# Kernel tuning notes

Measured on AMD Instinct MI355X. Metric: run time of the kernel, lower is better.

## Reference

```python
import jax, jax.numpy as jnp
import numpy as np

B, LQ, LKV = 4, 512, 8192
Q_DIM, KV_DIM = 1024, 512
QK_CH, V_CH, N_HEADS = 256, 256, 8
EPS = 1e-5


def _layernorm(x, g, b):
    m = jnp.mean(x, axis=-1, keepdims=True)
    v = jnp.mean(jnp.square(x - m), axis=-1, keepdims=True)
    return (x - m) * jax.lax.rsqrt(v + EPS) * g + b


def setup_inputs() -> dict:
    key = jax.random.key(0)
    ks = jax.random.split(key, 8)
    hidden_states = jax.random.normal(ks[0], (B, LQ, Q_DIM), dtype=jnp.float32)
    inputs = jax.random.normal(ks[1], (B, LKV, KV_DIM), dtype=jnp.float32)
    # Linear weights stored as [in, out] for x @ W
    Wq = jax.random.normal(ks[2], (Q_DIM, QK_CH), dtype=jnp.float32) * (1.0 / np.sqrt(Q_DIM))
    Wk = jax.random.normal(ks[3], (KV_DIM, QK_CH), dtype=jnp.float32) * (1.0 / np.sqrt(KV_DIM))
    Wv = jax.random.normal(ks[4], (KV_DIM, V_CH), dtype=jnp.float32) * (1.0 / np.sqrt(KV_DIM))
    bq = jnp.zeros((QK_CH,), jnp.float32)
    bk = jax.random.normal(ks[5], (QK_CH,), dtype=jnp.float32) * 0.02
    bv = jax.random.normal(ks[6], (V_CH,), dtype=jnp.float32) * 0.02
    ln1_g = jnp.ones((Q_DIM,), jnp.float32)
    ln1_b = jnp.zeros((Q_DIM,), jnp.float32)
    ln2_g = jnp.ones((KV_DIM,), jnp.float32)
    ln2_b = jnp.zeros((KV_DIM,), jnp.float32)
    return dict(hidden_states=hidden_states, inputs=inputs,
                ln1_g=ln1_g, ln1_b=ln1_b, ln2_g=ln2_g, ln2_b=ln2_b,
                Wq=Wq, bq=bq, Wk=Wk, bk=bk, Wv=Wv, bv=bv)


def reference(hidden_states, inputs, ln1_g, ln1_b, ln2_g, ln2_b,
              Wq, bq, Wk, bk, Wv, bv):
    H = N_HEADS
    dqk = QK_CH // H
    dv = V_CH // H
    hs = _layernorm(hidden_states, ln1_g, ln1_b)          # [B,LQ,Q_DIM]
    inp = _layernorm(inputs, ln2_g, ln2_b)                # [B,LKV,KV_DIM]
    q = (hs @ Wq + bq).reshape(B, LQ, H, dqk)             # [B,LQ,H,dqk]
    k = (inp @ Wk + bk).reshape(B, LKV, H, dqk)           # [B,LKV,H,dqk]
    v = (inp @ Wv + bv).reshape(B, LKV, H, dv)            # [B,LKV,H,dv]
    scores = jnp.einsum('bqhd,bkhd->bhqk', q, k) / np.sqrt(dqk).astype(np.float32)
    probs = jax.nn.softmax(scores, axis=-1)               # [B,H,LQ,LKV] (materialized, as in torch)
    ctx = jnp.einsum('bhqk,bkhd->bqhd', probs, v)         # [B,LQ,H,dv]
    return ctx.reshape(B, LQ, H * dv)
```

## Files before the change

### kernel.cpp

```cpp
#include <hip/hip_runtime.h>
#include <hip/hip_bf16.h>
#include <math.h>

#define NB    4
#define LQ    512
#define LKV   8192
#define QDIM  1024
#define KVDIM 512
#define NH    8
#define EPS_LN 1e-5f
#define SMAX  12.0f

typedef __attribute__((ext_vector_type(8))) short bf16x8;
typedef __attribute__((ext_vector_type(4))) float f32x4;

static __device__ __forceinline__ ushort f2bf(float x) {
    unsigned int u = __builtin_bit_cast(unsigned int, x);
    u += 0x7FFFu + ((u >> 16) & 1u);
    return (ushort)(u >> 16);
}

#if __has_builtin(__builtin_amdgcn_cvt_pk_bf16_f32)
static __device__ __forceinline__ unsigned int pk_bf16(float a, float b) {
    auto r = __builtin_amdgcn_cvt_pk_bf16_f32(a, b);
    return __builtin_bit_cast(unsigned int, r);
}
#else
static __device__ __forceinline__ unsigned int pk_bf16(float a, float b) {
    return (unsigned int)f2bf(a) | ((unsigned int)f2bf(b) << 16);
}
#endif

#if __has_builtin(__builtin_amdgcn_exp2f)
#define EXP2F(x) __builtin_amdgcn_exp2f(x)
#else
#define EXP2F(x) exp2f(x)
#endif

static __device__ __forceinline__ void gld_lds16(const ushort* g, ushort* l) {
    __builtin_amdgcn_global_load_lds(
        (const __attribute__((address_space(1))) unsigned int*)g,
        (__attribute__((address_space(3))) unsigned int*)l, 16, 0, 0);
}

static __device__ __forceinline__ void wt_transpose_body(
    const float* __restrict__ src, ushort* __restrict__ dst, int K,
    int kx, int ny, int t, ushort (*Ts)[72])
{
    const int k0 = kx * 64, n0 = ny * 64;
    const int nl = t & 63;
#pragma unroll
    for (int p = 0; p < 16; ++p) {
        const int kl = p * 4 + (t >> 6);
        Ts[nl][kl] = f2bf(src[(size_t)(k0 + kl) * 256 + n0 + nl]);
    }
    __syncthreads();
    const int ck = (t & 7) * 8;
#pragma unroll
    for (int p = 0; p < 2; ++p) {
        const int rn = p * 32 + (t >> 3);
        *(bf16x8*)(dst + (size_t)(n0 + rn) * K + k0 + ck) = *(const bf16x8*)&Ts[rn][ck];
    }
}

__global__ __launch_bounds__(256) void phaseA_kernel(
    const float* __restrict__ inputs, float* __restrict__ mean_i, float* __restrict__ rstd_i,
    const float* __restrict__ hidden, float* __restrict__ mean_h, float* __restrict__ rstd_h,
    const float* __restrict__ Wq, const float* __restrict__ Wk, const float* __restrict__ Wv,
    ushort* __restrict__ WtQ, ushort* __restrict__ WtKV)
{
    __shared__ ushort Ts[64][72];
    const int bid = blockIdx.x;
    const int t = threadIdx.x;
    const int lane = t & 63;
    if (bid < 8192) {
        const int row = bid * 4 + (t >> 6);
        const float* xp = inputs + (size_t)row * KVDIM;
        float s = 0.f, ss = 0.f;
#pragma unroll
        for (int i = 0; i < 2; ++i) {
            const float4 v = *(const float4*)(xp + lane * 4 + i * 256);
            s  += (v.x + v.y) + (v.z + v.w);
            ss += (v.x * v.x + v.y * v.y) + (v.z * v.z + v.w * v.w);
        }
#pragma unroll
        for (int o = 1; o < 64; o <<= 1) { s += __shfl_xor(s, o, 64); ss += __shfl_xor(ss, o, 64); }
        if (lane == 0) {
            const float mu = s * (1.0f / KVDIM);
            mean_i[row] = mu;
            rstd_i[row] = rsqrtf(ss * (1.0f / KVDIM) - mu * mu + EPS_LN);
        }
    } else if (bid < 8704) {
        const int row = (bid - 8192) * 4 + (t >> 6);
        const float* xp = hidden + (size_t)row * QDIM;
        float s = 0.f, ss = 0.f;
#pragma unroll
        for (int i = 0; i < 4; ++i) {
            const float4 v = *(const float4*)(xp + lane * 4 + i * 256);
            s  += (v.x + v.y) + (v.z + v.w);
            ss += (v.x * v.x + v.y * v.y) + (v.z * v.z + v.w * v.w);
        }
#pragma unroll
        for (int o = 1; o < 64; o <<= 1) { s += __shfl_xor(s, o, 64); ss += __shfl_xor(ss, o, 64); }
        if (lane == 0) {
            const float mu = s * (1.0f / QDIM);
            mean_h[row] = mu;
            rstd_h[row] = rsqrtf(ss * (1.0f / QDIM) - mu * mu + EPS_LN);
        }
    } else if (bid < 8768) {
        const int p = bid - 8704;
        wt_transpose_body(Wq, WtQ, QDIM, p & 15, p >> 4, t, Ts);
    } else if (bid < 8800) {
        const int p = bid - 8768;
        wt_transpose_body(Wk, WtKV, KVDIM, p & 7, p >> 3, t, Ts);
    } else {
        const int p = bid - 8800;
        wt_transpose_body(Wv, WtKV + (size_t)256 * KVDIM, KVDIM, p & 7, p >> 3, t, Ts);
    }
}

__global__ __launch_bounds__(256) void phaseB_kernel(
    const float* __restrict__ inputs,
    const float* __restrict__ mean_i, const float* __restrict__ rstd_i,
    const float* __restrict__ ln2g, const float* __restrict__ ln2b,
    const ushort* __restrict__ WtKV,
    const float* __restrict__ bk, const float* __restrict__ bv,
    ushort* __restrict__ kb, ushort* __restrict__ vt,
    const float* __restrict__ hidden,
    const float* __restrict__ mean_h, const float* __restrict__ rstd_h,
    const float* __restrict__ ln1g, const float* __restrict__ ln1b,
    const ushort* __restrict__ WtQ, const float* __restrict__ bq,
    ushort* __restrict__ qb, float oscale)
{
    __shared__ __align__(16) ushort SMEM[4 * 64 * 72];
    const int bid  = blockIdx.x;
    const int t    = threadIdx.x;
    const int lane = t & 63;
    const int w    = t >> 6;
    const int lq   = lane & 15;
    const int lg   = lane >> 4;
    const int wm   = w >> 1;
    const int wn   = w & 1;

    if (bid < 1024) {
        const int x  = bid & 7;
        const int j  = bid >> 3;
        const int bm = (x * 32 + (j >> 2)) * 128;
        const int bn = (j & 3) * 128;
        ushort* As = SMEM;
        ushort* Bs = SMEM + 4096;

        const int srow = t >> 2;
        const int scol = ((t & 3) ^ ((t >> 3) & 3)) * 8;
        const ushort* gB = WtKV + (size_t)(bn + srow) * KVDIM + scol;
        ushort* lB  = Bs + t * 8;
        ushort* lA0 = As + t * 8;
        ushort* lA1 = As + 2048 + t * 8;

        const int r0 = bm + srow;
        const float rs0 = rstd_i[r0],      mr0 = -mean_i[r0] * rs0;
        const float rs1 = rstd_i[r0 + 64], mr1 = -mean_i[r0 + 64] * rs1;
        const float* xp0 = inputs + (size_t)r0 * KVDIM + scol;
        const float* xp1 = xp0 + (size_t)64 * KVDIM;

        float4 a0 = *(const float4*)(xp0);
        float4 a1 = *(const float4*)(xp0 + 4);
        float4 c0 = *(const float4*)(xp1);
        float4 c1 = *(const float4*)(xp1 + 4);
        float4 g0 = *(const float4*)(ln2g + scol);
        float4 g1 = *(const float4*)(ln2g + scol + 4);
        float4 e0 = *(const float4*)(ln2b + scol);
        float4 e1 = *(const float4*)(ln2b + scol + 4);

        f32x4 acc[4][4] = {};
        for (int k0 = 0; k0 < KVDIM; k0 += 32) {
            gld_lds16(gB + k0,                       lB);
            gld_lds16(gB + (size_t)64 * KVDIM + k0,  lB + 2048);
            uint4 w0, w1;
            w0.x = pk_bf16(fmaf(fmaf(a0.x, rs0, mr0), g0.x, e0.x), fmaf(fmaf(a0.y, rs0, mr0), g0.y, e0.y));
            w0.y = pk_bf16(fmaf(fmaf(a0.z, rs0, mr0), g0.z, e0.z), fmaf(fmaf(a0.w, rs0, mr0), g0.w, e0.w));
            w0.z = pk_bf16(fmaf(fmaf(a1.x, rs0, mr0), g1.x, e1.x), fmaf(fmaf(a1.y, rs0, mr0), g1.y, e1.y));
            w0.w = pk_bf16(fmaf(fmaf(a1.z, rs0, mr0), g1.z, e1.z), fmaf(fmaf(a1.w, rs0, mr0), g1.w, e1.w));
            w1.x = pk_bf16(fmaf(fmaf(c0.x, rs1, mr1), g0.x, e0.x), fmaf(fmaf(c0.y, rs1, mr1), g0.y, e0.y));
            w1.y = pk_bf16(fmaf(fmaf(c0.z, rs1, mr1), g0.z, e0.z), fmaf(fmaf(c0.w, rs1, mr1), g0.w, e0.w));
            w1.z = pk_bf16(fmaf(fmaf(c1.x, rs1, mr1), g1.x, e1.x), fmaf(fmaf(c1.y, rs1, mr1), g1.y, e1.y));
            w1.w = pk_bf16(fmaf(fmaf(c1.z, rs1, mr1), g1.z, e1.z), fmaf(fmaf(c1.w, rs1, mr1), g1.w, e1.w));
            *(uint4*)lA0 = w0;
            *(uint4*)lA1 = w1;
            const int nk = (k0 + 32 < KVDIM) ? k0 + 32 : 0;
            a0 = *(const float4*)(xp0 + nk);
            a1 = *(const float4*)(xp0 + nk + 4);
            c0 = *(const float4*)(xp1 + nk);
            c1 = *(const float4*)(xp1 + nk + 4);
            g0 = *(const float4*)(ln2g + nk + scol);
            g1 = *(const float4*)(ln2g + nk + scol + 4);
            e0 = *(const float4*)(ln2b + nk + scol);
            e1 = *(const float4*)(ln2b + nk + scol + 4);
            __syncthreads();
            bf16x8 af[4], bf[4];
#pragma unroll
            for (int mt = 0; mt < 4; ++mt) {
                const int m = wm * 64 + mt * 16 + lq;
                af[mt] = *(const bf16x8*)(As + m * 32 + ((lg ^ ((m >> 1) & 3)) << 3));
            }
#pragma unroll
            for (int nt = 0; nt < 4; ++nt) {
                const int n = wn * 64 + nt * 16 + lq;
                bf[nt] = *(const bf16x8*)(Bs + n * 32 + ((lg ^ ((n >> 1) & 3)) << 3));
            }
#pragma unroll
            for (int mt = 0; mt < 4; ++mt)
#pragma unroll
                for (int nt = 0; nt < 4; ++nt)
                    acc[mt][nt] = __builtin_amdgcn_mfma_f32_16x16x32_bf16(af[mt], bf[nt], acc[mt][nt], 0, 0, 0);
            __syncthreads();
        }

        const int m0base = bm + wm * 64;
        const int bidx   = m0base >> 13;
        const int tokb   = m0base & 8191;

        if (bn < 256) {
            ushort (*Cs)[72] = (ushort(*)[72])(SMEM + w * 64 * 72);
#pragma unroll
            for (int nt = 0; nt < 4; ++nt) {
                const int n_l = nt * 16 + lq;
                const float bias = bk[bn + wn * 64 + n_l];
#pragma unroll
                for (int mt = 0; mt < 4; ++mt)
#pragma unroll
                    for (int r = 0; r < 4; ++r)
                        Cs[mt * 16 + lg * 4 + r][n_l] = f2bf(acc[mt][nt][r] + bias);
            }
            const int r0_ = lane >> 3;
            const int ck  = (lane & 7) * 8;
            const int nc  = bn + wn * 64 + ck;
            const int h = nc >> 5, d = nc & 31;
            const size_t obase = (((size_t)(bidx * NH + h) << 13) + tokb) * 32 + d;
#pragma unroll
            for (int p = 0; p < 8; ++p) {
                const int row = p * 8 + r0_;
                *(bf16x8*)(kb + obase + (size_t)row * 32) = *(const bf16x8*)&Cs[row][ck];
            }
        } else {
            ushort (*Cs)[72] = (ushort(*)[72])(SMEM + w * 64 * 72);
#pragma unroll
            for (int nt = 0; nt < 4; ++nt) {
                const int n_l = nt * 16 + lq;
                const float bias = bv[(bn - 256) + wn * 64 + n_l];
#pragma unroll
                for (int mt = 0; mt < 4; ++mt) {
                    uint2 o;
                    o.x = pk_bf16(acc[mt][nt][0] + bias, acc[mt][nt][1] + bias);
                    o.y = pk_bf16(acc[mt][nt][2] + bias, acc[mt][nt][3] + bias);
                    *(uint2*)&Cs[n_l][mt * 16 + lg * 4] = o;
                }
            }
            const int r0_ = lane >> 3;
            const int cm  = (lane & 7) * 8;
            const int tokc = tokb + cm;
#pragma unroll
            for (int p = 0; p < 8; ++p) {
                const int row = p * 8 + r0_;
                const int nv  = (bn - 256) + wn * 64 + row;
                const int h = nv >> 5, d = nv & 31;
                *(bf16x8*)(vt + ((size_t)(bidx * NH + h) * 32 + d) * LKV + tokc) =
                    *(const bf16x8*)&Cs[row][cm];
            }
        }
    } else {
        const int p  = bid - 1024;
        const int x  = p & 7;
        const int j  = p >> 3;
        const int bm = (x * 8 + (j >> 2)) * 32;
        const int bn = (j & 3) * 64;
        ushort* As = SMEM;
        ushort* Bs = SMEM + 2048;

        const int srow = t >> 3;
        const int scol = ((t & 7) ^ (srow & 7)) * 8;
        const ushort* gB = WtQ + (size_t)(bn + srow) * QDIM + scol;
        ushort* lB = Bs + t * 8;
        ushort* lA = As + t * 8;

        const int r = bm + srow;
        const float rs0 = rstd_h[r], mr0 = -mean_h[r] * rs0;
        const float* xA = hidden + (size_t)r * QDIM + scol;

        float4 a0 = *(const float4*)(xA);
        float4 a1 = *(const float4*)(xA + 4);
        float4 g0 = *(const float4*)(ln1g + scol);
        float4 g1 = *(const float4*)(ln1g + scol + 4);
        float4 e0 = *(const float4*)(ln1b + scol);
        float4 e1 = *(const float4*)(ln1b + scol + 4);

        f32x4 acc[2] = {};
        for (int k0 = 0; k0 < QDIM; k0 += 64) {
            gld_lds16(gB + k0,                      lB);
            gld_lds16(gB + (size_t)32 * QDIM + k0,  lB + 2048);
            uint4 w0;
            w0.x = pk_bf16(fmaf(fmaf(a0.x, rs0, mr0), g0.x, e0.x), fmaf(fmaf(a0.y, rs0, mr0), g0.y, e0.y));
            w0.y = pk_bf16(fmaf(fmaf(a0.z, rs0, mr0), g0.z, e0.z), fmaf(fmaf(a0.w, rs0, mr0), g0.w, e0.w));
            w0.z = pk_bf16(fmaf(fmaf(a1.x, rs0, mr0), g1.x, e1.x), fmaf(fmaf(a1.y, rs0, mr0), g1.y, e1.y));
            w0.w = pk_bf16(fmaf(fmaf(a1.z, rs0, mr0), g1.z, e1.z), fmaf(fmaf(a1.w, rs0, mr0), g1.w, e1.w));
            *(uint4*)lA = w0;
            const int nk = (k0 + 64 < QDIM) ? k0 + 64 : 0;
            a0 = *(const float4*)(xA + nk);
            a1 = *(const float4*)(xA + nk + 4);
            g0 = *(const float4*)(ln1g + nk + scol);
            g1 = *(const float4*)(ln1g + nk + scol + 4);
            e0 = *(const float4*)(ln1b + nk + scol);
            e1 = *(const float4*)(ln1b + nk + scol + 4);
            __syncthreads();
#pragma unroll
            for (int kh = 0; kh < 2; ++kh) {
                const int m = wm * 16 + lq;
                const bf16x8 af = *(const bf16x8*)(As + m * 64 + (((lg + 4 * kh) ^ (m & 7)) << 3));
#pragma unroll
                for (int nt = 0; nt < 2; ++nt) {
                    const int n = wn * 32 + nt * 16 + lq;
                    const bf16x8 bf = *(const bf16x8*)(Bs + n * 64 + (((lg + 4 * kh) ^ (n & 7)) << 3));
                    acc[nt] = __builtin_amdgcn_mfma_f32_16x16x32_bf16(af, bf, acc[nt], 0, 0, 0);
                }
            }
            __syncthreads();
        }

#pragma unroll
        for (int nt = 0; nt < 2; ++nt) {
            const int n = bn + wn * 32 + nt * 16 + lq;
            const int h = n >> 5, d = n & 31;
            const float bias = bq[n];
            const int m0   = bm + wm * 16 + lg * 4;
            const int bidx = m0 >> 9;
            const int tok  = m0 & 511;
            const size_t base = (((size_t)(bidx * NH + h) << 9) + tok) * 32 + d;
#pragma unroll
            for (int rr_ = 0; rr_ < 4; ++rr_)
                qb[base + (size_t)rr_ * 32] = f2bf((acc[nt][rr_] + bias) * oscale);
        }
    }
}

__global__ __launch_bounds__(512, 4) void attn_mfma_kernel(
    const ushort* __restrict__ Qb,
    const ushort* __restrict__ Kb,
    const ushort* __restrict__ Vt,
    float* __restrict__ Out)
{
    const int bid = blockIdx.x;
    const int xcd = bid & 7;
    const int rr  = bid >> 3;
    const int bh  = ((rr & 3) << 3) | xcd;
    const int qt  = rr >> 2;
    const int b = bh >> 3, h = bh & 7;
    const int t = threadIdx.x, w = t >> 6, lane = t & 63;
    const int lq = lane & 15, lg = lane >> 4;

    __shared__ __align__(16) ushort Pb[2][8][32][40];
    __shared__ float lbuf[8][32];

    bf16x8 qfrag[2];
    const size_t qbase = ((size_t)bh * LQ + qt * 32) * 32;
    qfrag[0] = *(const bf16x8*)(Qb + qbase + (size_t)lq * 32 + lg * 8);
    qfrag[1] = *(const bf16x8*)(Qb + qbase + (size_t)(16 + lq) * 32 + lg * 8);

    const ushort* KpA = Kb + ((size_t)bh * LKV + w * 1024 + lq) * 32 + lg * 8;
    const ushort* VpA = Vt + ((size_t)bh * 32 + lq) * LKV + w * 1024 + lg * 8;

    f32x4 oacc[2][2] = {};
    float l_part[2] = {0.f, 0.f};
    const f32x4 cM = {-SMAX, -SMAX, -SMAX, -SMAX};

    ushort* P0 = &Pb[0][w][0][0];
    ushort* P1 = &Pb[1][w][0][0];

    bf16x8 kf0 = *(const bf16x8*)(KpA);
    bf16x8 kf1 = *(const bf16x8*)(KpA + 16 * 32);
    bf16x8 vf0 = *(const bf16x8*)(VpA);
    bf16x8 vf1 = *(const bf16x8*)(VpA + (size_t)16 * LKV);

    bf16x8 vp0, vp1;

#define ATTN_EXPW(Pdst, s00, s10, s01, s11)                                              \
    do {                                                                                 \
        float p0, p1, p2, p3; uint2 pw;                                                  \
        p0 = EXP2F((s00)[0]); p1 = EXP2F((s00)[1]); p2 = EXP2F((s00)[2]); p3 = EXP2F((s00)[3]); \
        l_part[0] += (p0 + p1) + (p2 + p3);                                              \
        pw.x = pk_bf16(p0, p1); pw.y = pk_bf16(p2, p3);                                  \
        *(uint2*)((Pdst) + (lq) * 40 + lg * 4) = pw;                                     \
        p0 = EXP2F((s10)[0]); p1 = EXP2F((s10)[1]); p2 = EXP2F((s10)[2]); p3 = EXP2F((s10)[3]); \
        l_part[0] += (p0 + p1) + (p2 + p3);                                              \
        pw.x = pk_bf16(p0, p1); pw.y = pk_bf16(p2, p3);                                  \
        *(uint2*)((Pdst) + (lq) * 40 + 16 + lg * 4) = pw;                                \
        p0 = EXP2F((s01)[0]); p1 = EXP2F((s01)[1]); p2 = EXP2F((s01)[2]); p3 = EXP2F((s01)[3]); \
        l_part[1] += (p0 + p1) + (p2 + p3);                                              \
        pw.x = pk_bf16(p0, p1); pw.y = pk_bf16(p2, p3);                                  \
        *(uint2*)((Pdst) + (16 + lq) * 40 + lg * 4) = pw;                                \
        p0 = EXP2F((s11)[0]); p1 = EXP2F((s11)[1]); p2 = EXP2F((s11)[2]); p3 = EXP2F((s11)[3]); \
        l_part[1] += (p0 + p1) + (p2 + p3);                                              \
        pw.x = pk_bf16(p0, p1); pw.y = pk_bf16(p2, p3);                                  \
        *(uint2*)((Pdst) + (16 + lq) * 40 + 16 + lg * 4) = pw;                           \
    } while (0)

    {
        const bf16x8 kc0 = kf0, kc1 = kf1;
        vp0 = vf0; vp1 = vf1;
        kf0 = *(const bf16x8*)(KpA + (size_t)32 * 32);
        kf1 = *(const bf16x8*)(KpA + (size_t)48 * 32);
        vf0 = *(const bf16x8*)(VpA + 32);
        vf1 = *(const bf16x8*)(VpA + (size_t)16 * LKV + 32);
        f32x4 s00 = __builtin_amdgcn_mfma_f32_16x16x32_bf16(kc0, qfrag[0], cM, 0, 0, 0);
        f32x4 s01 = __builtin_amdgcn_mfma_f32_16x16x32_bf16(kc0, qfrag[1], cM, 0, 0, 0);
        f32x4 s10 = __builtin_amdgcn_mfma_f32_16x16x32_bf16(kc1, qfrag[0], cM, 0, 0, 0);
        f32x4 s11 = __builtin_amdgcn_mfma_f32_16x16x32_bf16(kc1, qfrag[1], cM, 0, 0, 0);
        ATTN_EXPW(P0, s00, s10, s01, s11);
    }

    for (int kt = 32; kt < 1024; kt += 32) {
        ushort* Pw = (kt & 32) ? P1 : P0;
        ushort* Pr = (kt & 32) ? P0 : P1;
        const bf16x8 kc0 = kf0, kc1 = kf1, vc0 = vf0, vc1 = vf1;
        const int nk = (kt + 32 < 1024) ? kt + 32 : 0;
        kf0 = *(const bf16x8*)(KpA + (size_t)nk * 32);
        kf1 = *(const bf16x8*)(KpA + (size_t)(nk + 16) * 32);
        vf0 = *(const bf16x8*)(VpA + nk);
        vf1 = *(const bf16x8*)(VpA + (size_t)16 * LKV + nk);

        f32x4 s00 = __builtin_amdgcn_mfma_f32_16x16x32_bf16(kc0, qfrag[0], cM, 0, 0, 0);
        f32x4 s01 = __builtin_amdgcn_mfma_f32_16x16x32_bf16(kc0, qfrag[1], cM, 0, 0, 0);
        f32x4 s10 = __builtin_amdgcn_mfma_f32_16x16x32_bf16(kc1, qfrag[0], cM, 0, 0, 0);
        f32x4 s11 = __builtin_amdgcn_mfma_f32_16x16x32_bf16(kc1, qfrag[1], cM, 0, 0, 0);

        const bf16x8 pf0 = *(const bf16x8*)(Pr + (size_t)lq * 40 + lg * 8);
        const bf16x8 pf1 = *(const bf16x8*)(Pr + (size_t)(16 + lq) * 40 + lg * 8);
        oacc[0][0] = __builtin_amdgcn_mfma_f32_16x16x32_bf16(vp0, pf0, oacc[0][0], 0, 0, 0);
        oacc[0][1] = __builtin_amdgcn_mfma_f32_16x16x32_bf16(vp0, pf1, oacc[0][1], 0, 0, 0);
        oacc[1][0] = __builtin_amdgcn_mfma_f32_16x16x32_bf16(vp1, pf0, oacc[1][0], 0, 0, 0);
        oacc[1][1] = __builtin_amdgcn_mfma_f32_16x16x32_bf16(vp1, pf1, oacc[1][1], 0, 0, 0);
        vp0 = vc0; vp1 = vc1;

        ATTN_EXPW(Pw, s00, s10, s01, s11);
    }

    {
        const bf16x8 pf0 = *(const bf16x8*)(P1 + (size_t)lq * 40 + lg * 8);
        const bf16x8 pf1 = *(const bf16x8*)(P1 + (size_t)(16 + lq) * 40 + lg * 8);
        oacc[0][0] = __builtin_amdgcn_mfma_f32_16x16x32_bf16(vp0, pf0, oacc[0][0], 0, 0, 0);
        oacc[0][1] = __builtin_amdgcn_mfma_f32_16x16x32_bf16(vp0, pf1, oacc[0][1], 0, 0, 0);
        oacc[1][0] = __builtin_amdgcn_mfma_f32_16x16x32_bf16(vp1, pf0, oacc[1][0], 0, 0, 0);
        oacc[1][1] = __builtin_amdgcn_mfma_f32_16x16x32_bf16(vp1, pf1, oacc[1][1], 0, 0, 0);
    }
#undef ATTN_EXPW

#pragma unroll
    for (int n = 0; n < 2; ++n) {
        l_part[n] += __shfl_xor(l_part[n], 16);
        l_part[n] += __shfl_xor(l_part[n], 32);
    }
    if (lg == 0) {
        lbuf[w][lq]      = l_part[0];
        lbuf[w][16 + lq] = l_part[1];
    }
    __syncthreads();

    float* Ob = (float*)&Pb[0][0][0][0];
    if (w >= 4) {
#pragma unroll
        for (int n = 0; n < 2; ++n)
#pragma unroll
            for (int dt = 0; dt < 2; ++dt)
                *(f32x4*)&Ob[((size_t)(w - 4) * 32 + n * 16 + lq) * 36 + dt * 16 + lg * 4] = oacc[dt][n];
    }
    __syncthreads();
    if (w < 4) {
#pragma unroll
        for (int n = 0; n < 2; ++n)
#pragma unroll
            for (int dt = 0; dt < 2; ++dt) {
                float* p = &Ob[((size_t)w * 32 + n * 16 + lq) * 36 + dt * 16 + lg * 4];
                f32x4 v = *(f32x4*)p;
                v += oacc[dt][n];
                *(f32x4*)p = v;
            }
    }
    __syncthreads();
    {
        const int q  = t >> 4;
        const int d0 = (t & 15) * 2;
        float s0 = 0.f, s1 = 0.f;
#pragma unroll
        for (int j = 0; j < 4; ++j) {
            s0 += Ob[((size_t)j * 32 + q) * 36 + d0];
            s1 += Ob[((size_t)j * 32 + q) * 36 + d0 + 1];
        }
        float gl = 0.f;
#pragma unroll
        for (int j = 0; j < 8; ++j) gl += lbuf[j][q];
        const float inv = 1.0f / gl;
        float2 o; o.x = s0 * inv; o.y = s1 * inv;
        *(float2*)(Out + ((size_t)b * LQ + qt * 32 + q) * 256 + h * 32 + d0) = o;
    }
}

extern "C" void kernel_launch(void* const* d_in, const int* in_sizes, int n_in,
                              void* d_out, int out_size, void* d_ws, size_t ws_size,
                              hipStream_t stream)
{
    const float* hidden = (const float*)d_in[0];
    const float* inputs = (const float*)d_in[1];
    const float* ln1g   = (const float*)d_in[2];
    const float* ln1b   = (const float*)d_in[3];
    const float* ln2g   = (const float*)d_in[4];
    const float* ln2b   = (const float*)d_in[5];
    const float* Wq     = (const float*)d_in[6];
    const float* bq     = (const float*)d_in[7];
    const float* Wk     = (const float*)d_in[8];
    const float* bk     = (const float*)d_in[9];
    const float* Wv     = (const float*)d_in[10];
    const float* bv     = (const float*)d_in[11];
    float* out = (float*)d_out;

    char* wsb = (char*)d_ws;
    ushort* qb     = (ushort*)(wsb);
    ushort* WtKV   = (ushort*)(wsb + (1u << 20));
    ushort* WtQ    = (ushort*)(wsb + (1u << 20) + (512u << 10));
    float*  mean_i = (float*)(wsb + (2u << 20));
    float*  rstd_i = (float*)(wsb + (2u << 20) + (128u << 10));
    float*  mean_h = (float*)(wsb + (2u << 20) + (256u << 10));
    float*  rstd_h = (float*)(wsb + (2u << 20) + (264u << 10));
    ushort* kb     = (ushort*)(wsb + (2u << 20) + (512u << 10));
    ushort* vt     = (ushort*)(wsb + (18u << 20) + (512u << 10));

    const float oscale = 0.2550540226496112f;

    phaseA_kernel<<<8832, 256, 0, stream>>>(inputs, mean_i, rstd_i,
                                            hidden, mean_h, rstd_h,
                                            Wq, Wk, Wv, WtQ, WtKV);
    phaseB_kernel<<<1280, 256, 0, stream>>>(inputs, mean_i, rstd_i, ln2g, ln2b,
                                            WtKV, bk, bv, kb, vt,
                                            hidden, mean_h, rstd_h, ln1g, ln1b,
                                            WtQ, bq, qb, oscale);
    attn_mfma_kernel<<<512, 512, 0, stream>>>(qb, kb, vt, out);
}
```

Baseline: 218.9 us.

## Fold LayerNorm affine into weights, double-buffer projection GEMMs, shuffle P in registers

LayerNorm gamma is folded into the transposed bf16 weights, and beta is folded into precomputed biases, so the projection GEMMs only apply mean/rstd normalization. Both projection GEMMs now double-buffer A and B tiles in LDS and overlap the next loads with MFMA, and the Q-projection blocks are scheduled first. The attention kernel drops the LDS round-trip for probabilities and builds the P operand with cross-lane shuffles, removing the one-step software pipeline. The tradeoffs are extra shuffle/select instructions, serial bias-fold loops in three single blocks, and slightly different rounding because gamma is applied before the bf16 conversion.

New measurement: 233.6 us. +6.7%, slower.

```diff
diff --git a/kernel.cpp b/kernel.cpp
--- a/kernel.cpp
+++ b/kernel.cpp
@@ -44,15 +44,15 @@
 }
 
 static __device__ __forceinline__ void wt_transpose_body(
-    const float* __restrict__ src, ushort* __restrict__ dst, int K,
-    int kx, int ny, int t, ushort (*Ts)[72])
+    const float* __restrict__ src, const float* __restrict__ g,
+    ushort* __restrict__ dst, int K, int kx, int ny, int t, ushort (*Ts)[72])
 {
     const int k0 = kx * 64, n0 = ny * 64;
     const int nl = t & 63;
 #pragma unroll
     for (int p = 0; p < 16; ++p) {
         const int kl = p * 4 + (t >> 6);
-        Ts[nl][kl] = f2bf(src[(size_t)(k0 + kl) * 256 + n0 + nl]);
+        Ts[nl][kl] = f2bf(g[k0 + kl] * src[(size_t)(k0 + kl) * 256 + n0 + nl]);
     }
     __syncthreads();
     const int ck = (t & 7) * 8;
@@ -67,7 +67,11 @@
     const float* __restrict__ inputs, float* __restrict__ mean_i, float* __restrict__ rstd_i,
     const float* __restrict__ hidden, float* __restrict__ mean_h, float* __restrict__ rstd_h,
     const float* __restrict__ Wq, const float* __restrict__ Wk, const float* __restrict__ Wv,
-    ushort* __restrict__ WtQ, ushort* __restrict__ WtKV)
+    const float* __restrict__ ln1g, const float* __restrict__ ln1b,
+    const float* __restrict__ ln2g, const float* __restrict__ ln2b,
+    const float* __restrict__ bq, const float* __restrict__ bk, const float* __restrict__ bv,
+    ushort* __restrict__ WtQ, ushort* __restrict__ WtKV,
+    float* __restrict__ bqF, float* __restrict__ bkF, float* __restrict__ bvF)
 {
     __shared__ ushort Ts[64][72];
     const int bid = blockIdx.x;
@@ -109,27 +113,37 @@
         }
     } else if (bid < 8768) {
         const int p = bid - 8704;
-        wt_transpose_body(Wq, WtQ, QDIM, p & 15, p >> 4, t, Ts);
+        wt_transpose_body(Wq, ln1g, WtQ, QDIM, p & 15, p >> 4, t, Ts);
     } else if (bid < 8800) {
         const int p = bid - 8768;
-        wt_transpose_body(Wk, WtKV, KVDIM, p & 7, p >> 3, t, Ts);
+        wt_transpose_body(Wk, ln2g, WtKV, KVDIM, p & 7, p >> 3, t, Ts);
+    } else if (bid < 8832) {
+        const int p = bid - 8800;
+        wt_transpose_body(Wv, ln2g, WtKV + (size_t)256 * KVDIM, KVDIM, p & 7, p >> 3, t, Ts);
+    } else if (bid == 8832) {
+        float s = bk[t];
+        for (int k = 0; k < KVDIM; ++k) s += ln2b[k] * Wk[(size_t)k * 256 + t];
+        bkF[t] = s;
+    } else if (bid == 8833) {
+        float s = bv[t];
+        for (int k = 0; k < KVDIM; ++k) s += ln2b[k] * Wv[(size_t)k * 256 + t];
+        bvF[t] = s;
     } else {
-        const int p = bid - 8800;
-        wt_transpose_body(Wv, WtKV + (size_t)256 * KVDIM, KVDIM, p & 7, p >> 3, t, Ts);
+        float s = bq[t];
+        for (int k = 0; k < QDIM; ++k) s += ln1b[k] * Wq[(size_t)k * 256 + t];
+        bqF[t] = s;
     }
 }
 
 __global__ __launch_bounds__(256) void phaseB_kernel(
     const float* __restrict__ inputs,
     const float* __restrict__ mean_i, const float* __restrict__ rstd_i,
-    const float* __restrict__ ln2g, const float* __restrict__ ln2b,
     const ushort* __restrict__ WtKV,
-    const float* __restrict__ bk, const float* __restrict__ bv,
+    const float* __restrict__ bkF, const float* __restrict__ bvF,
     ushort* __restrict__ kb, ushort* __restrict__ vt,
     const float* __restrict__ hidden,
     const float* __restrict__ mean_h, const float* __restrict__ rstd_h,
-    const float* __restrict__ ln1g, const float* __restrict__ ln1b,
-    const ushort* __restrict__ WtQ, const float* __restrict__ bq,
+    const ushort* __restrict__ WtQ, const float* __restrict__ bqF,
     ushort* __restrict__ qb, float oscale)
 {
     __shared__ __align__(16) ushort SMEM[4 * 64 * 72];
@@ -142,20 +156,16 @@
     const int wm   = w >> 1;
     const int wn   = w & 1;
 
-    if (bid < 1024) {
-        const int x  = bid & 7;
-        const int j  = bid >> 3;
+    if (bid >= 256) {
+        const int kid = bid - 256;
+        const int x  = kid & 7;
+        const int j  = kid >> 3;
         const int bm = (x * 32 + (j >> 2)) * 128;
         const int bn = (j & 3) * 128;
-        ushort* As = SMEM;
-        ushort* Bs = SMEM + 4096;
 
         const int srow = t >> 2;
         const int scol = ((t & 3) ^ ((t >> 3) & 3)) * 8;
         const ushort* gB = WtKV + (size_t)(bn + srow) * KVDIM + scol;
-        ushort* lB  = Bs + t * 8;
-        ushort* lA0 = As + t * 8;
-        ushort* lA1 = As + 2048 + t * 8;
 
         const int r0 = bm + srow;
         const float rs0 = rstd_i[r0],      mr0 = -mean_i[r0] * rs0;
@@ -163,56 +173,72 @@
         const float* xp0 = inputs + (size_t)r0 * KVDIM + scol;
         const float* xp1 = xp0 + (size_t)64 * KVDIM;
 
+        f32x4 acc[4][4] = {};
+
+        gld_lds16(gB + 0,                      SMEM + 8192 + t * 8);
+        gld_lds16(gB + (size_t)64 * KVDIM + 0, SMEM + 8192 + 2048 + t * 8);
         float4 a0 = *(const float4*)(xp0);
         float4 a1 = *(const float4*)(xp0 + 4);
         float4 c0 = *(const float4*)(xp1);
         float4 c1 = *(const float4*)(xp1 + 4);
-        float4 g0 = *(const float4*)(ln2g + scol);
-        float4 g1 = *(const float4*)(ln2g + scol + 4);
-        float4 e0 = *(const float4*)(ln2b + scol);
-        float4 e1 = *(const float4*)(ln2b + scol + 4);
-
-        f32x4 acc[4][4] = {};
-        for (int k0 = 0; k0 < KVDIM; k0 += 32) {
-            gld_lds16(gB + k0,                       lB);
-            gld_lds16(gB + (size_t)64 * KVDIM + k0,  lB + 2048);
+        {
             uint4 w0, w1;
-            w0.x = pk_bf16(fmaf(fmaf(a0.x, rs0, mr0), g0.x, e0.x), fmaf(fmaf(a0.y, rs0, mr0), g0.y, e0.y));
-            w0.y = pk_bf16(fmaf(fmaf(a0.z, rs0, mr0), g0.z, e0.z), fmaf(fmaf(a0.w, rs0, mr0), g0.w, e0.w));
-            w0.z = pk_bf16(fmaf(fmaf(a1.x, rs0, mr0), g1.x, e1.x), fmaf(fmaf(a1.y, rs0, mr0), g1.y, e1.y));
-            w0.w = pk_bf16(fmaf(fmaf(a1.z, rs0, mr0), g1.z, e1.z), fmaf(fmaf(a1.w, rs0, mr0), g1.w, e1.w));
-            w1.x = pk_bf16(fmaf(fmaf(c0.x, rs1, mr1), g0.x, e0.x), fmaf(fmaf(c0.y, rs1, mr1), g0.y, e0.y));
-            w1.y = pk_bf16(fmaf(fmaf(c0.z, rs1, mr1), g0.z, e0.z), fmaf(fmaf(c0.w, rs1, mr1), g0.w, e0.w));
-            w1.z = pk_bf16(fmaf(fmaf(c1.x, rs1, mr1), g1.x, e1.x), fmaf(fmaf(c1.y, rs1, mr1), g1.y, e1.y));
-            w1.w = pk_bf16(fmaf(fmaf(c1.z, rs1, mr1), g1.z, e1.z), fmaf(fmaf(c1.w, rs1, mr1), g1.w, e1.w));
-            *(uint4*)lA0 = w0;
-            *(uint4*)lA1 = w1;
-            const int nk = (k0 + 32 < KVDIM) ? k0 + 32 : 0;
-            a0 = *(const float4*)(xp0 + nk);
-            a1 = *(const float4*)(xp0 + nk + 4);
-            c0 = *(const float4*)(xp1 + nk);
-            c1 = *(const float4*)(xp1 + nk + 4);
-            g0 = *(const float4*)(ln2g + nk + scol);
-            g1 = *(const float4*)(ln2g + nk + scol + 4);
-            e0 = *(const float4*)(ln2b + nk + scol);
-            e1 = *(const float4*)(ln2b + nk + scol + 4);
-            __syncthreads();
+            w0.x = pk_bf16(fmaf(a0.x, rs0, mr0), fmaf(a0.y, rs0, mr0));
+            w0.y = pk_bf16(fmaf(a0.z, rs0, mr0), fmaf(a0.w, rs0, mr0));
+            w0.z = pk_bf16(fmaf(a1.x, rs0, mr0), fmaf(a1.y, rs0, mr0));
+            w0.w = pk_bf16(fmaf(a1.z, rs0, mr0), fmaf(a1.w, rs0, mr0));
+            w1.x = pk_bf16(fmaf(c0.x, rs1, mr1), fmaf(c0.y, rs1, mr1));
+            w1.y = pk_bf16(fmaf(c0.z, rs1, mr1), fmaf(c0.w, rs1, mr1));
+            w1.z = pk_bf16(fmaf(c1.x, rs1, mr1), fmaf(c1.y, rs1, mr1));
+            w1.w = pk_bf16(fmaf(c1.z, rs1, mr1), fmaf(c1.w, rs1, mr1));
+            *(uint4*)(SMEM + t * 8) = w0;
+            *(uint4*)(SMEM + 2048 + t * 8) = w1;
+        }
+        __syncthreads();
+
+        for (int i = 0; i < 16; ++i) {
+            const int co = (i & 1) * 4096;
+            const int no = 4096 - co;
+            ushort* Asc = SMEM + co;
+            ushort* Bsc = SMEM + 8192 + co;
+            ushort* Asn = SMEM + no;
+            ushort* Bsn = SMEM + 8192 + no;
+            const int kn = (i + 1 < 16) ? (i + 1) * 32 : 0;
+            gld_lds16(gB + kn,                      Bsn + t * 8);
+            gld_lds16(gB + (size_t)64 * KVDIM + kn, Bsn + 2048 + t * 8);
+            a0 = *(const float4*)(xp0 + kn);
+            a1 = *(const float4*)(xp0 + kn + 4);
+            c0 = *(const float4*)(xp1 + kn);
+            c1 = *(const float4*)(xp1 + kn + 4);
+
             bf16x8 af[4], bf[4];
 #pragma unroll
             for (int mt = 0; mt < 4; ++mt) {
                 const int m = wm * 64 + mt * 16 + lq;
-                af[mt] = *(const bf16x8*)(As + m * 32 + ((lg ^ ((m >> 1) & 3)) << 3));
+                af[mt] = *(const bf16x8*)(Asc + m * 32 + ((lg ^ ((m >> 1) & 3)) << 3));
             }
 #pragma unroll
             for (int nt = 0; nt < 4; ++nt) {
                 const int n = wn * 64 + nt * 16 + lq;
-                bf[nt] = *(const bf16x8*)(Bs + n * 32 + ((lg ^ ((n >> 1) & 3)) << 3));
+                bf[nt] = *(const bf16x8*)(Bsc + n * 32 + ((lg ^ ((n >> 1) & 3)) << 3));
             }
 #pragma unroll
             for (int mt = 0; mt < 4; ++mt)
 #pragma unroll
                 for (int nt = 0; nt < 4; ++nt)
                     acc[mt][nt] = __builtin_amdgcn_mfma_f32_16x16x32_bf16(af[mt], bf[nt], acc[mt][nt], 0, 0, 0);
+
+            uint4 w0, w1;
+            w0.x = pk_bf16(fmaf(a0.x, rs0, mr0), fmaf(a0.y, rs0, mr0));
+            w0.y = pk_bf16(fmaf(a0.z, rs0, mr0), fmaf(a0.w, rs0, mr0));
+            w0.z = pk_bf16(fmaf(a1.x, rs0, mr0), fmaf(a1.y, rs0, mr0));
+            w0.w = pk_bf16(fmaf(a1.z, rs0, mr0), fmaf(a1.w, rs0, mr0));
+            w1.x = pk_bf16(fmaf(c0.x, rs1, mr1), fmaf(c0.y, rs1, mr1));
+            w1.y = pk_bf16(fmaf(c0.z, rs1, mr1), fmaf(c0.w, rs1, mr1));
+            w1.z = pk_bf16(fmaf(c1.x, rs1, mr1), fmaf(c1.y, rs1, mr1));
+            w1.w = pk_bf16(fmaf(c1.z, rs1, mr1), fmaf(c1.w, rs1, mr1));
+            *(uint4*)(Asn + t * 8) = w0;
+            *(uint4*)(Asn + 2048 + t * 8) = w1;
             __syncthreads();
         }
 
@@ -225,7 +251,7 @@
 #pragma unroll
             for (int nt = 0; nt < 4; ++nt) {
                 const int n_l = nt * 16 + lq;
-                const float bias = bk[bn + wn * 64 + n_l];
+                const float bias = bkF[bn + wn * 64 + n_l];
 #pragma unroll
                 for (int mt = 0; mt < 4; ++mt)
 #pragma unroll
@@ -247,7 +273,7 @@
 #pragma unroll
             for (int nt = 0; nt < 4; ++nt) {
                 const int n_l = nt * 16 + lq;
-                const float bias = bv[(bn - 256) + wn * 64 + n_l];
+                const float bias = bvF[(bn - 256) + wn * 64 + n_l];
 #pragma unroll
                 for (int mt = 0; mt < 4; ++mt) {
                     uint2 o;
@@ -269,60 +295,67 @@
             }
         }
     } else {
-        const int p  = bid - 1024;
-        const int x  = p & 7;
-        const int j  = p >> 3;
+        const int x  = bid & 7;
+        const int j  = bid >> 3;
         const int bm = (x * 8 + (j >> 2)) * 32;
         const int bn = (j & 3) * 64;
-        ushort* As = SMEM;
-        ushort* Bs = SMEM + 2048;
 
         const int srow = t >> 3;
         const int scol = ((t & 7) ^ (srow & 7)) * 8;
         const ushort* gB = WtQ + (size_t)(bn + srow) * QDIM + scol;
-        ushort* lB = Bs + t * 8;
-        ushort* lA = As + t * 8;
 
         const int r = bm + srow;
         const float rs0 = rstd_h[r], mr0 = -mean_h[r] * rs0;
         const float* xA = hidden + (size_t)r * QDIM + scol;
 
+        f32x4 acc[2] = {};
+
+        gld_lds16(gB + 0,                     SMEM + 4096 + t * 8);
+        gld_lds16(gB + (size_t)32 * QDIM + 0, SMEM + 4096 + 2048 + t * 8);
         float4 a0 = *(const float4*)(xA);
         float4 a1 = *(const float4*)(xA + 4);
-        float4 g0 = *(const float4*)(ln1g + scol);
-        float4 g1 = *(const float4*)(ln1g + scol + 4);
-        float4 e0 = *(const float4*)(ln1b + scol);
-        float4 e1 = *(const float4*)(ln1b + scol + 4);
-
-        f32x4 acc[2] = {};
-        for (int k0 = 0; k0 < QDIM; k0 += 64) {
-            gld_lds16(gB + k0,                      lB);
-            gld_lds16(gB + (size_t)32 * QDIM + k0,  lB + 2048);
+        {
             uint4 w0;
-            w0.x = pk_bf16(fmaf(fmaf(a0.x, rs0, mr0), g0.x, e0.x), fmaf(fmaf(a0.y, rs0, mr0), g0.y, e0.y));
-            w0.y = pk_bf16(fmaf(fmaf(a0.z, rs0, mr0), g0.z, e0.z), fmaf(fmaf(a0.w, rs0, mr0), g0.w, e0.w));
-            w0.z = pk_bf16(fmaf(fmaf(a1.x, rs0, mr0), g1.x, e1.x), fmaf(fmaf(a1.y, rs0, mr0), g1.y, e1.y));
-            w0.w = pk_bf16(fmaf(fmaf(a1.z, rs0, mr0), g1.z, e1.z), fmaf(fmaf(a1.w, rs0, mr0), g1.w, e1.w));
-            *(uint4*)lA = w0;
-            const int nk = (k0 + 64 < QDIM) ? k0 + 64 : 0;
-            a0 = *(const float4*)(xA + nk);
-            a1 = *(const float4*)(xA + nk + 4);
-            g0 = *(const float4*)(ln1g + nk + scol);
-            g1 = *(const float4*)(ln1g + nk + scol + 4);
-            e0 = *(const float4*)(ln1b + nk + scol);
-            e1 = *(const float4*)(ln1b + nk + scol + 4);
-            __syncthreads();
+            w0.x = pk_bf16(fmaf(a0.x, rs0, mr0), fmaf(a0.y, rs0, mr0));
+            w0.y = pk_bf16(fmaf(a0.z, rs0, mr0), fmaf(a0.w, rs0, mr0));
+            w0.z = pk_bf16(fmaf(a1.x, rs0, mr0), fmaf(a1.y, rs0, mr0));
+            w0.w = pk_bf16(fmaf(a1.z, rs0, mr0), fmaf(a1.w, rs0, mr0));
+            *(uint4*)(SMEM + t * 8) = w0;
+        }
+        __syncthreads();
+
+        for (int i = 0; i < 16; ++i) {
+            const int ca = (i & 1) * 2048;
+            const int na = 2048 - ca;
+            const int cb = (i & 1) * 4096;
+            const int nb = 4096 - cb;
+            ushort* Asc = SMEM + ca;
+            ushort* Bsc = SMEM + 4096 + cb;
+            ushort* Asn = SMEM + na;
+            ushort* Bsn = SMEM + 4096 + nb;
+            const int kn = (i + 1 < 16) ? (i + 1) * 64 : 0;
+            gld_lds16(gB + kn,                     Bsn + t * 8);
+            gld_lds16(gB + (size_t)32 * QDIM + kn, Bsn + 2048 + t * 8);
+            a0 = *(const float4*)(xA + kn);
+            a1 = *(const float4*)(xA + kn + 4);
+
 #pragma unroll
             for (int kh = 0; kh < 2; ++kh) {
                 const int m = wm * 16 + lq;
-                const bf16x8 af = *(const bf16x8*)(As + m * 64 + (((lg + 4 * kh) ^ (m & 7)) << 3));
+                const bf16x8 af = *(const bf16x8*)(Asc + m * 64 + (((lg + 4 * kh) ^ (m & 7)) << 3));
 #pragma unroll
                 for (int nt = 0; nt < 2; ++nt) {
                     const int n = wn * 32 + nt * 16 + lq;
-                    const bf16x8 bf = *(const bf16x8*)(Bs + n * 64 + (((lg + 4 * kh) ^ (n & 7)) << 3));
+                    const bf16x8 bf = *(const bf16x8*)(Bsc + n * 64 + (((lg + 4 * kh) ^ (n & 7)) << 3));
                     acc[nt] = __builtin_amdgcn_mfma_f32_16x16x32_bf16(af, bf, acc[nt], 0, 0, 0);
                 }
             }
+            uint4 w0;
+            w0.x = pk_bf16(fmaf(a0.x, rs0, mr0), fmaf(a0.y, rs0, mr0));
+            w0.y = pk_bf16(fmaf(a0.z, rs0, mr0), fmaf(a0.w, rs0, mr0));
+            w0.z = pk_bf16(fmaf(a1.x, rs0, mr0), fmaf(a1.y, rs0, mr0));
+            w0.w = pk_bf16(fmaf(a1.z, rs0, mr0), fmaf(a1.w, rs0, mr0));
+            *(uint4*)(Asn + t * 8) = w0;
             __syncthreads();
         }
 
@@ -330,7 +363,7 @@
         for (int nt = 0; nt < 2; ++nt) {
             const int n = bn + wn * 32 + nt * 16 + lq;
             const int h = n >> 5, d = n & 31;
-            const float bias = bq[n];
+            const float bias = bqF[n];
             const int m0   = bm + wm * 16 + lg * 4;
             const int bidx = m0 >> 9;
             const int tok  = m0 & 511;
@@ -357,7 +390,7 @@
     const int t = threadIdx.x, w = t >> 6, lane = t & 63;
     const int lq = lane & 15, lg = lane >> 4;
 
-    __shared__ __align__(16) ushort Pb[2][8][32][40];
+    __shared__ float Ob[4][32][36];
     __shared__ float lbuf[8][32];
 
     bf16x8 qfrag[2];
@@ -372,54 +405,16 @@
     float l_part[2] = {0.f, 0.f};
     const f32x4 cM = {-SMAX, -SMAX, -SMAX, -SMAX};
 
-    ushort* P0 = &Pb[0][w][0][0];
-    ushort* P1 = &Pb[1][w][0][0];
+    const int srcA = lq + ((lg & 1) << 5);
+    const int srcB = srcA + 16;
+    const bool hi  = (lg >= 2);
 
     bf16x8 kf0 = *(const bf16x8*)(KpA);
     bf16x8 kf1 = *(const bf16x8*)(KpA + 16 * 32);
     bf16x8 vf0 = *(const bf16x8*)(VpA);
     bf16x8 vf1 = *(const bf16x8*)(VpA + (size_t)16 * LKV);
 
-    bf16x8 vp0, vp1;
-
-#define ATTN_EXPW(Pdst, s00, s10, s01, s11)                                              \
-    do {                                                                                 \
-        float p0, p1, p2, p3; uint2 pw;                                                  \
-        p0 = EXP2F((s00)[0]); p1 = EXP2F((s00)[1]); p2 = EXP2F((s00)[2]); p3 = EXP2F((s00)[3]); \
-        l_part[0] += (p0 + p1) + (p2 + p3);                                              \
-        pw.x = pk_bf16(p0, p1); pw.y = pk_bf16(p2, p3);                                  \
-        *(uint2*)((Pdst) + (lq) * 40 + lg * 4) = pw;                                     \
-        p0 = EXP2F((s10)[0]); p1 = EXP2F((s10)[1]); p2 = EXP2F((s10)[2]); p3 = EXP2F((s10)[3]); \
-        l_part[0] += (p0 + p1) + (p2 + p3);                                              \
-        pw.x = pk_bf16(p0, p1); pw.y = pk_bf16(p2, p3);                                  \
-        *(uint2*)((Pdst) + (lq) * 40 + 16 + lg * 4) = pw;                                \
-        p0 = EXP2F((s01)[0]); p1 = EXP2F((s01)[1]); p2 = EXP2F((s01)[2]); p3 = EXP2F((s01)[3]); \
-        l_part[1] += (p0 + p1) + (p2 + p3);                                              \
-        pw.x = pk_bf16(p0, p1); pw.y = pk_bf16(p2, p3);                                  \
-        *(uint2*)((Pdst) + (16 + lq) * 40 + lg * 4) = pw;                                \
-        p0 = EXP2F((s11)[0]); p1 = EXP2F((s11)[1]); p2 = EXP2F((s11)[2]); p3 = EXP2F((s11)[3]); \
-        l_part[1] += (p0 + p1) + (p2 + p3);                                              \
-        pw.x = pk_bf16(p0, p1); pw.y = pk_bf16(p2, p3);                                  \
-        *(uint2*)((Pdst) + (16 + lq) * 40 + 16 + lg * 4) = pw;                           \
-    } while (0)
-
-    {
-        const bf16x8 kc0 = kf0, kc1 = kf1;
-        vp0 = vf0; vp1 = vf1;
-        kf0 = *(const bf16x8*)(KpA + (size_t)32 * 32);
-        kf1 = *(const bf16x8*)(KpA + (size_t)48 * 32);
-        vf0 = *(const bf16x8*)(VpA + 32);
-        vf1 = *(const bf16x8*)(VpA + (size_t)16 * LKV + 32);
-        f32x4 s00 = __builtin_amdgcn_mfma_f32_16x16x32_bf16(kc0, qfrag[0], cM, 0, 0, 0);
-        f32x4 s01 = __builtin_amdgcn_mfma_f32_16x16x32_bf16(kc0, qfrag[1], cM, 0, 0, 0);
-        f32x4 s10 = __builtin_amdgcn_mfma_f32_16x16x32_bf16(kc1, qfrag[0], cM, 0, 0, 0);
-        f32x4 s11 = __builtin_amdgcn_mfma_f32_16x16x32_bf16(kc1, qfrag[1], cM, 0, 0, 0);
-        ATTN_EXPW(P0, s00, s10, s01, s11);
-    }
-
-    for (int kt = 32; kt < 1024; kt += 32) {
-        ushort* Pw = (kt & 32) ? P1 : P0;
-        ushort* Pr = (kt & 32) ? P0 : P1;
+    for (int kt = 0; kt < 1024; kt += 32) {
         const bf16x8 kc0 = kf0, kc1 = kf1, vc0 = vf0, vc1 = vf1;
         const int nk = (kt + 32 < 1024) ? kt + 32 : 0;
         kf0 = *(const bf16x8*)(KpA + (size_t)nk * 32);
@@ -428,30 +423,41 @@
         vf1 = *(const bf16x8*)(VpA + (size_t)16 * LKV + nk);
 
         f32x4 s00 = __builtin_amdgcn_mfma_f32_16x16x32_bf16(kc0, qfrag[0], cM, 0, 0, 0);
+        f32x4 s10 = __builtin_amdgcn_mfma_f32_16x16x32_bf16(kc1, qfrag[0], cM, 0, 0, 0);
         f32x4 s01 = __builtin_amdgcn_mfma_f32_16x16x32_bf16(kc0, qfrag[1], cM, 0, 0, 0);
-        f32x4 s10 = __builtin_amdgcn_mfma_f32_16x16x32_bf16(kc1, qfrag[0], cM, 0, 0, 0);
         f32x4 s11 = __builtin_amdgcn_mfma_f32_16x16x32_bf16(kc1, qfrag[1], cM, 0, 0, 0);
 
-        const bf16x8 pf0 = *(const bf16x8*)(Pr + (size_t)lq * 40 + lg * 8);
-        const bf16x8 pf1 = *(const bf16x8*)(Pr + (size_t)(16 + lq) * 40 + lg * 8);
-        oacc[0][0] = __builtin_amdgcn_mfma_f32_16x16x32_bf16(vp0, pf0, oacc[0][0], 0, 0, 0);
-        oacc[0][1] = __builtin_amdgcn_mfma_f32_16x16x32_bf16(vp0, pf1, oacc[0][1], 0, 0, 0);
-        oacc[1][0] = __builtin_amdgcn_mfma_f32_16x16x32_bf16(vp1, pf0, oacc[1][0], 0, 0, 0);
-        oacc[1][1] = __builtin_amdgcn_mfma_f32_16x16x32_bf16(vp1, pf1, oacc[1][1], 0, 0, 0);
-        vp0 = vc0; vp1 = vc1;
-
-        ATTN_EXPW(Pw, s00, s10, s01, s11);
-    }
-
-    {
-        const bf16x8 pf0 = *(const bf16x8*)(P1 + (size_t)lq * 40 + lg * 8);
-        const bf16x8 pf1 = *(const bf16x8*)(P1 + (size_t)(16 + lq) * 40 + lg * 8);
-        oacc[0][0] = __builtin_amdgcn_mfma_f32_16x16x32_bf16(vp0, pf0, oacc[0][0], 0, 0, 0);
-        oacc[0][1] = __builtin_amdgcn_mfma_f32_16x16x32_bf16(vp0, pf1, oacc[0][1], 0, 0, 0);
-        oacc[1][0] = __builtin_amdgcn_mfma_f32_16x16x32_bf16(vp1, pf0, oacc[1][0], 0, 0, 0);
-        oacc[1][1] = __builtin_amdgcn_mfma_f32_16x16x32_bf16(vp1, pf1, oacc[1][1], 0, 0, 0);
-    }
-#undef ATTN_EXPW
+        bf16x8 pf[2];
+#pragma unroll
+        for (int n = 0; n < 2; ++n) {
+            const f32x4 sa = n ? s01 : s00;
+            const f32x4 sb = n ? s11 : s10;
+            const float p0 = EXP2F(sa[0]), p1 = EXP2F(sa[1]), p2 = EXP2F(sa[2]), p3 = EXP2F(sa[3]);
+            const float p4 = EXP2F(sb[0]), p5 = EXP2F(sb[1]), p6 = EXP2F(sb[2]), p7 = EXP2F(sb[3]);
+            l_part[n] += ((p0 + p1) + (p2 + p3)) + ((p4 + p5) + (p6 + p7));
+            const unsigned int w0x = pk_bf16(p0, p1), w0y = pk_bf16(p2, p3);
+            const unsigned int w1x = pk_bf16(p4, p5), w1y = pk_bf16(p6, p7);
+            const unsigned int a0 = (unsigned int)__shfl((int)w0x, srcA, 64);
+            const unsigned int a1 = (unsigned int)__shfl((int)w0y, srcA, 64);
+            const unsigned int b0 = (unsigned int)__shfl((int)w1x, srcA, 64);
+            const unsigned int b1 = (unsigned int)__shfl((int)w1y, srcA, 64);
+            const unsigned int a2 = (unsigned int)__shfl((int)w0x, srcB, 64);
+            const unsigned int a3 = (unsigned int)__shfl((int)w0y, srcB, 64);
+            const unsigned int b2 = (unsigned int)__shfl((int)w1x, srcB, 64);
+            const unsigned int b3 = (unsigned int)__shfl((int)w1y, srcB, 64);
+            uint4 u;
+            u.x = hi ? b0 : a0;
+            u.y = hi ? b1 : a1;
+            u.z = hi ? b2 : a2;
+            u.w = hi ? b3 : a3;
+            pf[n] = __builtin_bit_cast(bf16x8, u);
+        }
+
+        oacc[0][0] = __builtin_amdgcn_mfma_f32_16x16x32_bf16(vc0, pf[0], oacc[0][0], 0, 0, 0);
+        oacc[0][1] = __builtin_amdgcn_mfma_f32_16x16x32_bf16(vc0, pf[1], oacc[0][1], 0, 0, 0);
+        oacc[1][0] = __builtin_amdgcn_mfma_f32_16x16x32_bf16(vc1, pf[0], oacc[1][0], 0, 0, 0);
+        oacc[1][1] = __builtin_amdgcn_mfma_f32_16x16x32_bf16(vc1, pf[1], oacc[1][1], 0, 0, 0);
+    }
 
 #pragma unroll
     for (int n = 0; n < 2; ++n) {
@@ -462,15 +468,13 @@
         lbuf[w][lq]      = l_part[0];
         lbuf[w][16 + lq] = l_part[1];
     }
-    __syncthreads();
-
-    float* Ob = (float*)&Pb[0][0][0][0];
+
     if (w >= 4) {
 #pragma unroll
         for (int n = 0; n < 2; ++n)
 #pragma unroll
             for (int dt = 0; dt < 2; ++dt)
-                *(f32x4*)&Ob[((size_t)(w - 4) * 32 + n * 16 + lq) * 36 + dt * 16 + lg * 4] = oacc[dt][n];
+                *(f32x4*)&Ob[w - 4][n * 16 + lq][dt * 16 + lg * 4] = oacc[dt][n];
     }
     __syncthreads();
     if (w < 4) {
@@ -478,7 +482,7 @@
         for (int n = 0; n < 2; ++n)
 #pragma unroll
             for (int dt = 0; dt < 2; ++dt) {
-                float* p = &Ob[((size_t)w * 32 + n * 16 + lq) * 36 + dt * 16 + lg * 4];
+                float* p = &Ob[w][n * 16 + lq][dt * 16 + lg * 4];
                 f32x4 v = *(f32x4*)p;
                 v += oacc[dt][n];
                 *(f32x4*)p = v;
@@ -491,8 +495,8 @@
         float s0 = 0.f, s1 = 0.f;
 #pragma unroll
         for (int j = 0; j < 4; ++j) {
-            s0 += Ob[((size_t)j * 32 + q) * 36 + d0];
-            s1 += Ob[((size_t)j * 32 + q) * 36 + d0 + 1];
+            s0 += Ob[j][q][d0];
+            s1 += Ob[j][q][d0 + 1];
         }
         float gl = 0.f;
 #pragma unroll
@@ -529,17 +533,22 @@
     float*  rstd_i = (float*)(wsb + (2u << 20) + (128u << 10));
     float*  mean_h = (float*)(wsb + (2u << 20) + (256u << 10));
     float*  rstd_h = (float*)(wsb + (2u << 20) + (264u << 10));
-    ushort* kb     = (ushort*)(wsb + (2u << 20) + (512u << 10));
-    ushort* vt     = (ushort*)(wsb + (18u << 20) + (512u << 10));
+    float*  bkF    = (float*)(wsb + (2u << 20) + (272u << 10));
+    float*  bvF    = (float*)(wsb + (2u << 20) + (273u << 10));
+    float*  bqF    = (float*)(wsb + (2u << 20) + (274u << 10));
+    ushort* kb     = (ushort*)(wsb + (3u << 20));
+    ushort* vt     = (ushort*)(wsb + (19u << 20));
 
     const float oscale = 0.2550540226496112f;
 
-    phaseA_kernel<<<8832, 256, 0, stream>>>(inputs, mean_i, rstd_i,
+    phaseA_kernel<<<8835, 256, 0, stream>>>(inputs, mean_i, rstd_i,
                                             hidden, mean_h, rstd_h,
-                                            Wq, Wk, Wv, WtQ, WtKV);
-    phaseB_kernel<<<1280, 256, 0, stream>>>(inputs, mean_i, rstd_i, ln2g, ln2b,
-                                            WtKV, bk, bv, kb, vt,
-                                            hidden, mean_h, rstd_h, ln1g, ln1b,
-                                            WtQ, bq, qb, oscale);
+                                            Wq, Wk, Wv, ln1g, ln1b, ln2g, ln2b,
+                                            bq, bk, bv,
+                                            WtQ, WtKV, bqF, bkF, bvF);
+    phaseB_kernel<<<1280, 256, 0, stream>>>(inputs, mean_i, rstd_i,
+                                            WtKV, bkF, bvF, kb, vt,
+                                            hidden, mean_h, rstd_h,
+                                            WtQ, bqF, qb, oscale);
     attn_mfma_kernel<<<512, 512, 0, stream>>>(qb, kb, vt, out);
 }
```
